# Performance work log

Measured on AMD Instinct MI355X. Metric: run time of the kernel, lower is better.

## Reference

```python
import jax, jax.numpy as jnp
import numpy as np

B, S, D, H, HD, NU, T = 64, 512, 256, 4, 64, 100000, 24


def setup_inputs() -> dict:
    key = jax.random.key(0)
    ks = jax.random.split(key, 13)
    return {
        "timeslot_embedded": jax.random.normal(ks[0], (T, D), jnp.float32),
        "user": jax.random.randint(ks[1], (B,), 0, NU, dtype=jnp.int64) if jax.config.jax_enable_x64 else jax.random.randint(ks[1], (B,), 0, NU, dtype=jnp.int32),
        "hour": jax.random.randint(ks[2], (B, S), 0, T, dtype=jnp.int32),
        "hour_mask": jax.random.randint(ks[3], (B, S, T), 0, 2, dtype=jnp.int32),
        "user_pref": jax.random.normal(ks[4], (NU, D), jnp.float32) * 0.02,
        "Wq": jax.random.normal(ks[5], (H, HD, 2 * D), jnp.float32) * 0.02,
        "bq": jnp.zeros((H, HD), jnp.float32),
        "Wk": jax.random.normal(ks[6], (H, HD, D), jnp.float32) * 0.02,
        "bk": jnp.zeros((H, HD), jnp.float32),
        "Wv": jax.random.normal(ks[7], (H, HD, D), jnp.float32) * 0.02,
        "bv": jnp.zeros((H, HD), jnp.float32),
        "Wu": jax.random.normal(ks[8], (D, D), jnp.float32) * 0.02,
        "bu": jnp.zeros((D,), jnp.float32),
    }


def reference(timeslot_embedded, user, hour, hour_mask, user_pref,
              Wq, bq, Wk, bk, Wv, bv, Wu, bu):
    b, s = hour.shape
    n = b * s
    # per-token features
    user_feat = jnp.broadcast_to(user_pref[user][:, None, :], (b, s, D)).reshape(n, D)
    time_feat = timeslot_embedded[hour.reshape(n)]          # [N, D]
    query = jnp.concatenate([user_feat, time_feat], axis=-1)  # [N, 2D]
    # all heads at once (equivalent to the per-head Linear loop)
    q = jnp.einsum('nd,hkd->nhk', query, Wq) + bq[None]               # [N, H, HD]
    k = jnp.einsum('td,hkd->htk', timeslot_embedded, Wk) + bk[:, None, :]  # [H, T, HD]
    v = jnp.einsum('td,hkd->htk', timeslot_embedded, Wv) + bv[:, None, :]  # [H, T, HD]
    scale = 1.0 / np.sqrt(HD).astype(np.float32)
    scores = jnp.einsum('nhk,htk->nht', q, k) * scale                 # [N, H, T]
    mask = hour_mask.reshape(n, T)[:, None, :]                        # [N, 1, T]
    scores = jnp.where(mask == 1, -jnp.inf, scores)
    attn = jax.nn.softmax(scores, axis=-1)
    out = jnp.einsum('nht,htk->nhk', attn, v).reshape(n, H * HD)      # concat heads
    out = out @ Wu.T + bu
    return out.reshape(b, s, D)
```

## Files before the change

kernel.cpp:

```cpp
#include <hip/hip_runtime.h>
#include <hip/hip_bf16.h>

#define QU_OFF   0
#define QT_OFF   16384
#define KK_OFF   22528
#define VV_OFF   28672
#define EU_OFF   34816
#define ET_OFF   40960
#define VWB_OFF  43264

typedef __attribute__((ext_vector_type(8))) short bf16x8;
typedef __attribute__((ext_vector_type(4))) float f32x4;

__device__ __forceinline__ unsigned short f2bf(float f) {
    unsigned u = __builtin_bit_cast(unsigned, f);
    return (unsigned short)((u + 0x7FFFu + ((u >> 16) & 1u)) >> 16);
}

__global__ __launch_bounds__(256) void precompA(
    const float* __restrict__ ts, const int* __restrict__ user,
    const float* __restrict__ user_pref,
    const float* __restrict__ Wq, const float* __restrict__ bq,
    const float* __restrict__ Wk, const float* __restrict__ bk,
    const float* __restrict__ Wv, const float* __restrict__ bv,
    float* __restrict__ ws)
{
    int tid = threadIdx.x;
    int lane = tid & 63;
    int gw = blockIdx.x * 4 + (tid >> 6);
    const float* wrow; const float* x; float bias = 0.f; float* outp;
    if (gw < 16384) {
        int b = gw >> 8, j = gw & 255;
        wrow = Wq + j * 512;
        x = user_pref + (long long)user[b] * 256;
        outp = ws + QU_OFF + gw;
    } else if (gw < 22528) {
        int r = gw - 16384, t = r >> 8, j = r & 255;
        wrow = Wq + j * 512 + 256; x = ts + t * 256; bias = bq[j];
        outp = ws + QT_OFF + r;
    } else if (gw < 28672) {
        int r = gw - 22528, t = r >> 8, j = r & 255;
        wrow = Wk + j * 256; x = ts + t * 256; bias = bk[j];
        outp = ws + KK_OFF + ((j >> 6) * 24 + t) * 64 + (j & 63);
    } else {
        int r = gw - 28672, t = r >> 8, j = r & 255;
        wrow = Wv + j * 256; x = ts + t * 256; bias = bv[j];
        outp = ws + VV_OFF + ((j >> 6) * 24 + t) * 64 + (j & 63);
    }
    float s = 0.f;
    #pragma unroll
    for (int i = 0; i < 4; ++i) s = fmaf(wrow[lane + 64 * i], x[lane + 64 * i], s);
    #pragma unroll
    for (int off = 32; off; off >>= 1) s += __shfl_xor(s, off);
    if (lane == 0) *outp = s + bias;
}

__global__ __launch_bounds__(256) void precompB(float* __restrict__ ws,
                                                const float* __restrict__ Wu)
{
    const float* qu = ws + QU_OFF;
    const float* qt = ws + QT_OFF;
    const float* kk = ws + KK_OFF;
    const float* vv = ws + VV_OFF;
    int o = blockIdx.x * 256 + threadIdx.x;
    if (o < 12288) {
        int htp = o >> 8, d = o & 255;
        int ht = htp * 2;
        int h = ht / 24;
        const float4* v0 = (const float4*)(vv + ht * 64);
        const float4* v1 = (const float4*)(vv + ht * 64 + 64);
        const float4* wp = (const float4*)(Wu + d * 256 + h * 64);
        float s0 = 0.f, s1 = 0.f;
        #pragma unroll
        for (int i = 0; i < 16; ++i) {
            float4 wv = wp[i], a = v0[i], c = v1[i];
            s0 = fmaf(a.x, wv.x, fmaf(a.y, wv.y, fmaf(a.z, wv.z, fmaf(a.w, wv.w, s0))));
            s1 = fmaf(c.x, wv.x, fmaf(c.y, wv.y, fmaf(c.z, wv.z, fmaf(c.w, wv.w, s1))));
        }
        int kt = ht >> 5, nt = d >> 4, lg = (ht >> 3) & 3, jh = (ht & 7) >> 1;
        unsigned pack = (unsigned)f2bf(s0) | ((unsigned)f2bf(s1) << 16);
        ((unsigned*)(ws + VWB_OFF))[(kt * 16 + nt) * 256 + ((d & 15) + 16 * lg) * 4 + jh] = pack;
    } else if (o < 18432) {
        int o2 = o - 12288;
        int b = o2 / 96, rem = o2 - b * 96;
        const float* qp = qu + b * 256 + (rem / 24) * 64;
        const float* kp = kk + rem * 64;
        float s = 0.f;
        #pragma unroll 8
        for (int hd = 0; hd < 64; ++hd) s = fmaf(qp[hd], kp[hd], s);
        ws[EU_OFF + o2] = expf(s * 0.125f);
    } else if (o < 20736) {
        int o3 = o - 18432;
        int tp = o3 / 96, rem = o3 - tp * 96;
        const float* qp = qt + tp * 256 + (rem / 24) * 64;
        const float* kp = kk + rem * 64;
        float s = 0.f;
        #pragma unroll 8
        for (int hd = 0; hd < 64; ++hd) s = fmaf(qp[hd], kp[hd], s);
        ws[ET_OFF + o3] = expf(s * 0.125f);
    }
}

__global__ __launch_bounds__(256) void attn_mfma(
    const int* __restrict__ hour, const int* __restrict__ hour_mask,
    const float* __restrict__ ws, const float* __restrict__ bu,
    float* __restrict__ out)
{
    const float* EU = ws + EU_OFF;
    const float* ET = ws + ET_OFF;
    __shared__ int4 A_lds[12 * 64];
    int tid = threadIdx.x;
    int nb = blockIdx.x * 64;
    int b = nb >> 9;
    {
        int tok = tid >> 2, h = tid & 3;
        int n = nb + tok;
        int th = hour[n];
        const float4* EUp = (const float4*)(EU + b * 96 + h * 24);
        const float4* ETp = (const float4*)(ET + th * 96 + h * 24);
        const int4*   mp  = (const int4*)(hour_mask + (long long)n * 24);
        float p[24]; float ssum = 0.f;
        #pragma unroll
        for (int q = 0; q < 6; ++q) {
            float4 e = EUp[q]; float4 f = ETp[q]; int4 m = mp[q];
            float v0 = (m.x != 0) ? 0.f : e.x * f.x;
            float v1 = (m.y != 0) ? 0.f : e.y * f.y;
            float v2 = (m.z != 0) ? 0.f : e.z * f.z;
            float v3 = (m.w != 0) ? 0.f : e.w * f.w;
            p[q*4+0] = v0; p[q*4+1] = v1; p[q*4+2] = v2; p[q*4+3] = v3;
            ssum += (v0 + v1) + (v2 + v3);
        }
        float r = 1.0f / ssum;
        int mt = tok >> 4, tl = tok & 15;
        #pragma unroll
        for (int tp = 0; tp < 12; ++tp) {
            int ht = h * 24 + tp * 2;
            unsigned pack = (unsigned)f2bf(p[tp*2] * r)
                          | ((unsigned)f2bf(p[tp*2+1] * r) << 16);
            int kt = ht >> 5, lg = (ht >> 3) & 3, jh = (ht & 7) >> 1;
            ((unsigned*)A_lds)[((kt * 4 + mt) * 64 + tl + 16 * lg) * 4 + jh] = pack;
        }
    }
    __syncthreads();
    int w = tid >> 6, l = tid & 63;
    const int4* Bg = (const int4*)(ws + VWB_OFF);
    bf16x8 afr[3][4], bfr[3][4];
    #pragma unroll
    for (int kt = 0; kt < 3; ++kt)
        #pragma unroll
        for (int q = 0; q < 4; ++q) {
            afr[kt][q] = __builtin_bit_cast(bf16x8, A_lds[(kt * 4 + q) * 64 + l]);
            bfr[kt][q] = __builtin_bit_cast(bf16x8, Bg[(kt * 16 + w * 4 + q) * 64 + l]);
        }
    f32x4 acc[4][4];
    #pragma unroll
    for (int mt = 0; mt < 4; ++mt)
        #pragma unroll
        for (int q = 0; q < 4; ++q) acc[mt][q] = (f32x4)0.f;
    #pragma unroll
    for (int kt = 0; kt < 3; ++kt)
        #pragma unroll
        for (int mt = 0; mt < 4; ++mt)
            #pragma unroll
            for (int q = 0; q < 4; ++q)
                acc[mt][q] = __builtin_amdgcn_mfma_f32_16x16x32_bf16(
                    afr[kt][mt], bfr[kt][q], acc[mt][q], 0, 0, 0);
    int colb = w * 64 + (l & 15);
    float buv[4];
    #pragma unroll
    for (int q = 0; q < 4; ++q) buv[q] = bu[colb + q * 16];
    int row0 = nb + (l >> 4) * 4;
    #pragma unroll
    for (int mt = 0; mt < 4; ++mt)
        #pragma unroll
        for (int q = 0; q < 4; ++q) {
            float* op = out + (size_t)(row0 + mt * 16) * 256 + colb + q * 16;
            #pragma unroll
            for (int r = 0; r < 4; ++r)
                op[(size_t)r * 256] = acc[mt][q][r] + buv[q];
        }
}

extern "C" void kernel_launch(void* const* d_in, const int* in_sizes, int n_in,
                              void* d_out, int out_size, void* d_ws, size_t ws_size,
                              hipStream_t stream)
{
    const float* ts        = (const float*)d_in[0];
    const int*   user      = (const int*)  d_in[1];
    const int*   hour      = (const int*)  d_in[2];
    const int*   hour_mask = (const int*)  d_in[3];
    const float* user_pref = (const float*)d_in[4];
    const float* Wq        = (const float*)d_in[5];
    const float* bq        = (const float*)d_in[6];
    const float* Wk        = (const float*)d_in[7];
    const float* bk        = (const float*)d_in[8];
    const float* Wv        = (const float*)d_in[9];
    const float* bv        = (const float*)d_in[10];
    const float* Wu        = (const float*)d_in[11];
    const float* bu        = (const float*)d_in[12];
    float* ws  = (float*)d_ws;
    float* out = (float*)d_out;

    hipLaunchKernelGGL(precompA, dim3(8704), dim3(256), 0, stream,
                       ts, user, user_pref, Wq, bq, Wk, bk, Wv, bv, ws);
    hipLaunchKernelGGL(precompB, dim3(81), dim3(256), 0, stream, ws, Wu);
    hipLaunchKernelGGL(attn_mfma, dim3(512), dim3(256), 0, stream,
                       hour, hour_mask, ws, bu, out);
}
```

Measured before the change: 26.12 us.

## Fuse precompute kernels into one MFMA-based kernel and compute EU in attention

Replaces the two precompute kernels (a wave-per-dot-product projection pass over 8704 blocks and a scalar follow-up) with a single 16-block kernel. It does the Q/K/V projections and the V·Wu product with bf16 MFMA, and computes the time-query exp scores in shared memory. The user-key exp scores move into the attention kernel, where each block computes its 96 values into LDS. This removes one launch and a lot of redundant global traffic. In exchange, the projections now run on only 16 blocks at bf16 precision, and each attention block repeats the EU computation.

```diff
diff --git a/kernel.cpp b/kernel.cpp
--- a/kernel.cpp
+++ b/kernel.cpp
@@ -2,12 +2,9 @@
 #include <hip/hip_bf16.h>
 
 #define QU_OFF   0
-#define QT_OFF   16384
-#define KK_OFF   22528
-#define VV_OFF   28672
-#define EU_OFF   34816
-#define ET_OFF   40960
-#define VWB_OFF  43264
+#define KK_OFF   16384
+#define ET_OFF   22528
+#define VWB_OFF  24832
 
 typedef __attribute__((ext_vector_type(8))) short bf16x8;
 typedef __attribute__((ext_vector_type(4))) float f32x4;
@@ -16,88 +13,210 @@
     unsigned u = __builtin_bit_cast(unsigned, f);
     return (unsigned short)((u + 0x7FFFu + ((u >> 16) & 1u)) >> 16);
 }
-
-__global__ __launch_bounds__(256) void precompA(
+__device__ __forceinline__ unsigned packbf(float a, float b) {
+    return (unsigned)f2bf(a) | ((unsigned)f2bf(b) << 16);
+}
+__device__ __forceinline__ bf16x8 cvt8(float4 f0, float4 f1) {
+    int4 v = make_int4(packbf(f0.x, f0.y), packbf(f0.z, f0.w),
+                       packbf(f1.x, f1.y), packbf(f1.z, f1.w));
+    return __builtin_bit_cast(bf16x8, v);
+}
+__device__ __forceinline__ float dot4(float4 a, float4 b, float s) {
+    return fmaf(a.x, b.x, fmaf(a.y, b.y, fmaf(a.z, b.z, fmaf(a.w, b.w, s))));
+}
+
+
+__global__ __launch_bounds__(256) void precomp(
     const float* __restrict__ ts, const int* __restrict__ user,
     const float* __restrict__ user_pref,
     const float* __restrict__ Wq, const float* __restrict__ bq,
     const float* __restrict__ Wk, const float* __restrict__ bk,
     const float* __restrict__ Wv, const float* __restrict__ bv,
-    float* __restrict__ ws)
+    const float* __restrict__ Wu, float* __restrict__ ws)
 {
-    int tid = threadIdx.x;
-    int lane = tid & 63;
-    int gw = blockIdx.x * 4 + (tid >> 6);
-    const float* wrow; const float* x; float bias = 0.f; float* outp;
-    if (gw < 16384) {
-        int b = gw >> 8, j = gw & 255;
-        wrow = Wq + j * 512;
-        x = user_pref + (long long)user[b] * 256;
-        outp = ws + QU_OFF + gw;
-    } else if (gw < 22528) {
-        int r = gw - 16384, t = r >> 8, j = r & 255;
-        wrow = Wq + j * 512 + 256; x = ts + t * 256; bias = bq[j];
-        outp = ws + QT_OFF + r;
-    } else if (gw < 28672) {
-        int r = gw - 22528, t = r >> 8, j = r & 255;
-        wrow = Wk + j * 256; x = ts + t * 256; bias = bk[j];
-        outp = ws + KK_OFF + ((j >> 6) * 24 + t) * 64 + (j & 63);
-    } else {
-        int r = gw - 28672, t = r >> 8, j = r & 255;
-        wrow = Wv + j * 256; x = ts + t * 256; bias = bv[j];
-        outp = ws + VV_OFF + ((j >> 6) * 24 + t) * 64 + (j & 63);
-    }
-    float s = 0.f;
-    #pragma unroll
-    for (int i = 0; i < 4; ++i) s = fmaf(wrow[lane + 64 * i], x[lane + 64 * i], s);
-    #pragma unroll
-    for (int off = 32; off; off >>= 1) s += __shfl_xor(s, off);
-    if (lane == 0) *outp = s + bias;
-}
-
-__global__ __launch_bounds__(256) void precompB(float* __restrict__ ws,
-                                                const float* __restrict__ Wu)
-{
-    const float* qu = ws + QU_OFF;
-    const float* qt = ws + QT_OFF;
-    const float* kk = ws + KK_OFF;
-    const float* vv = ws + VV_OFF;
-    int o = blockIdx.x * 256 + threadIdx.x;
-    if (o < 12288) {
-        int htp = o >> 8, d = o & 255;
-        int ht = htp * 2;
-        int h = ht / 24;
-        const float4* v0 = (const float4*)(vv + ht * 64);
-        const float4* v1 = (const float4*)(vv + ht * 64 + 64);
-        const float4* wp = (const float4*)(Wu + d * 256 + h * 64);
-        float s0 = 0.f, s1 = 0.f;
-        #pragma unroll
-        for (int i = 0; i < 16; ++i) {
-            float4 wv = wp[i], a = v0[i], c = v1[i];
-            s0 = fmaf(a.x, wv.x, fmaf(a.y, wv.y, fmaf(a.z, wv.z, fmaf(a.w, wv.w, s0))));
-            s1 = fmaf(c.x, wv.x, fmaf(c.y, wv.y, fmaf(c.z, wv.z, fmaf(c.w, wv.w, s1))));
-        }
-        int kt = ht >> 5, nt = d >> 4, lg = (ht >> 3) & 3, jh = (ht & 7) >> 1;
-        unsigned pack = (unsigned)f2bf(s0) | ((unsigned)f2bf(s1) << 16);
-        ((unsigned*)(ws + VWB_OFF))[(kt * 16 + nt) * 256 + ((d & 15) + 16 * lg) * 4 + jh] = pack;
-    } else if (o < 18432) {
-        int o2 = o - 12288;
-        int b = o2 / 96, rem = o2 - b * 96;
-        const float* qp = qu + b * 256 + (rem / 24) * 64;
-        const float* kp = kk + rem * 64;
-        float s = 0.f;
-        #pragma unroll 8
-        for (int hd = 0; hd < 64; ++hd) s = fmaf(qp[hd], kp[hd], s);
-        ws[EU_OFF + o2] = expf(s * 0.125f);
-    } else if (o < 20736) {
-        int o3 = o - 18432;
-        int tp = o3 / 96, rem = o3 - tp * 96;
-        const float* qp = qt + tp * 256 + (rem / 24) * 64;
-        const float* kp = kk + rem * 64;
-        float s = 0.f;
-        #pragma unroll 8
-        for (int hd = 0; hd < 64; ++hd) s = fmaf(qp[hd], kp[hd], s);
-        ws[ET_OFF + o3] = expf(s * 0.125f);
+    __shared__ unsigned sA[4096];
+    __shared__ float sM1[32 * 68];
+    __shared__ float sM2[32 * 68];
+    int tid = threadIdx.x, blk = blockIdx.x;
+    int w = tid >> 6, l = tid & 63;
+    int eo = (l >> 4) * 8;
+
+    if (blk < 8) {
+        int q = blk >> 1, nh = blk & 1, b0 = q * 16;
+        for (int u = tid; u < 512; u += 256) {
+            int r = u >> 5, e0 = (u & 31) * 8;
+            const float* src = user_pref + (size_t)user[b0 + r] * 256 + e0;
+            float4 f0 = *(const float4*)src, f1 = *(const float4*)(src + 4);
+            unsigned* dst = &sA[(((e0 >> 5) * 2) * 64 + (r & 15) + 16 * ((e0 >> 3) & 3)) * 4];
+            dst[0] = packbf(f0.x, f0.y); dst[1] = packbf(f0.z, f0.w);
+            dst[2] = packbf(f1.x, f1.y); dst[3] = packbf(f1.z, f1.w);
+        }
+        __syncthreads();
+        #pragma unroll
+        for (int ntq = 0; ntq < 2; ++ntq) {
+            int col = nh * 128 + (w * 2 + ntq) * 16 + (l & 15);
+            float4 fb[8][2];
+            #pragma unroll
+            for (int kt = 0; kt < 8; ++kt) {
+                const float* Bp = Wq + (size_t)col * 512 + kt * 32 + eo;
+                fb[kt][0] = *(const float4*)Bp; fb[kt][1] = *(const float4*)(Bp + 4);
+            }
+            f32x4 acc = (f32x4)0.f;
+            #pragma unroll
+            for (int kt = 0; kt < 8; ++kt) {
+                bf16x8 afr = __builtin_bit_cast(bf16x8, *(const int4*)&sA[((kt * 2) * 64 + l) * 4]);
+                acc = __builtin_amdgcn_mfma_f32_16x16x32_bf16(afr, cvt8(fb[kt][0], fb[kt][1]), acc, 0, 0, 0);
+            }
+            int row = (l >> 4) * 4;
+            #pragma unroll
+            for (int r = 0; r < 4; ++r)
+                ws[QU_OFF + (size_t)(b0 + row + r) * 256 + col] = acc[r];
+        }
+        return;
+    }
+
+    for (int u = tid; u < 768; u += 256) {
+        int r = u >> 5, e0 = (u & 31) * 8;
+        const float* src = ts + r * 256 + e0;
+        float4 f0 = *(const float4*)src, f1 = *(const float4*)(src + 4);
+        unsigned* dst = &sA[(((e0 >> 5) * 2 + (r >> 4)) * 64 + (r & 15) + 16 * ((e0 >> 3) & 3)) * 4];
+        dst[0] = packbf(f0.x, f0.y); dst[1] = packbf(f0.z, f0.w);
+        dst[2] = packbf(f1.x, f1.y); dst[3] = packbf(f1.z, f1.w);
+    }
+    __syncthreads();
+
+    if (blk < 12) {
+        int h = blk - 8;
+        int j = h * 64 + w * 16 + (l & 15);
+        float4 fa[8][2], fc[8][2];
+        #pragma unroll
+        for (int kt = 0; kt < 8; ++kt) {
+            const float* Bq = Wq + (size_t)j * 512 + 256 + kt * 32 + eo;
+            const float* Bk = Wk + (size_t)j * 256 + kt * 32 + eo;
+            fa[kt][0] = *(const float4*)Bq; fa[kt][1] = *(const float4*)(Bq + 4);
+            fc[kt][0] = *(const float4*)Bk; fc[kt][1] = *(const float4*)(Bk + 4);
+        }
+        f32x4 aca[2] = {(f32x4)0.f, (f32x4)0.f};
+        f32x4 acb[2] = {(f32x4)0.f, (f32x4)0.f};
+        #pragma unroll
+        for (int kt = 0; kt < 8; ++kt) {
+            bf16x8 bq8 = cvt8(fa[kt][0], fa[kt][1]);
+            bf16x8 bk8 = cvt8(fc[kt][0], fc[kt][1]);
+            #pragma unroll
+            for (int mt = 0; mt < 2; ++mt) {
+                bf16x8 afr = __builtin_bit_cast(bf16x8, *(const int4*)&sA[((kt * 2 + mt) * 64 + l) * 4]);
+                aca[mt] = __builtin_amdgcn_mfma_f32_16x16x32_bf16(afr, bq8, aca[mt], 0, 0, 0);
+                acb[mt] = __builtin_amdgcn_mfma_f32_16x16x32_bf16(afr, bk8, acb[mt], 0, 0, 0);
+            }
+        }
+        float bqv = bq[j], bkv = bk[j];
+        int hd = w * 16 + (l & 15);
+        #pragma unroll
+        for (int mt = 0; mt < 2; ++mt) {
+            int t0 = mt * 16 + (l >> 4) * 4;
+            #pragma unroll
+            for (int r = 0; r < 4; ++r) {
+                int t = t0 + r;
+                if (t < 24) {
+                    sM1[t * 68 + hd] = aca[mt][r] + bqv;
+                    float kv = acb[mt][r] + bkv;
+                    sM2[t * 68 + hd] = kv;
+                    ws[KK_OFF + (h * 24 + t) * 64 + hd] = kv;
+                }
+            }
+        }
+        __syncthreads();
+        for (int u = tid; u < 576; u += 256) {
+            int tp = u / 24, t = u - tp * 24;
+            const float4* qp4 = (const float4*)&sM1[tp * 68];
+            const float4* kp4 = (const float4*)&sM2[t * 68];
+            float s = 0.f;
+            #pragma unroll
+            for (int i = 0; i < 16; ++i) s = dot4(qp4[i], kp4[i], s);
+            ws[ET_OFF + tp * 96 + h * 24 + t] = expf(s * 0.125f);
+        }
+        return;
+    }
+
+    {
+        int h = blk - 12;
+        int jv = h * 64 + w * 16 + (l & 15);
+        float4 fv[8][2];
+        #pragma unroll
+        for (int kt = 0; kt < 8; ++kt) {
+            const float* Bv = Wv + (size_t)jv * 256 + kt * 32 + eo;
+            fv[kt][0] = *(const float4*)Bv; fv[kt][1] = *(const float4*)(Bv + 4);
+        }
+        f32x4 acv[2] = {(f32x4)0.f, (f32x4)0.f};
+        #pragma unroll
+        for (int kt = 0; kt < 8; ++kt) {
+            bf16x8 bv8 = cvt8(fv[kt][0], fv[kt][1]);
+            #pragma unroll
+            for (int mt = 0; mt < 2; ++mt) {
+                bf16x8 afr = __builtin_bit_cast(bf16x8, *(const int4*)&sA[((kt * 2 + mt) * 64 + l) * 4]);
+                acv[mt] = __builtin_amdgcn_mfma_f32_16x16x32_bf16(afr, bv8, acv[mt], 0, 0, 0);
+            }
+        }
+        float bvv = bv[jv];
+        int hd = w * 16 + (l & 15);
+        #pragma unroll
+        for (int mt = 0; mt < 2; ++mt) {
+            int t0 = mt * 16 + (l >> 4) * 4;
+            #pragma unroll
+            for (int r = 0; r < 4; ++r)
+                if (t0 + r < 24) sM1[(t0 + r) * 68 + hd] = acv[mt][r] + bvv;
+        }
+        __syncthreads();
+        f32x4 ac2[2][4];
+        #pragma unroll
+        for (int mt = 0; mt < 2; ++mt)
+            #pragma unroll
+            for (int q = 0; q < 4; ++q) ac2[mt][q] = (f32x4)0.f;
+        #pragma unroll
+        for (int kt2 = 0; kt2 < 2; ++kt2) {
+            int k0 = kt2 * 32 + eo;
+            bf16x8 a2[2];
+            #pragma unroll
+            for (int mt = 0; mt < 2; ++mt) {
+                int m = mt * 16 + (l & 15);
+                float4 g0 = *(const float4*)&sM1[m * 68 + k0];
+                float4 g1 = *(const float4*)&sM1[m * 68 + k0 + 4];
+                a2[mt] = cvt8(g0, g1);
+            }
+            float4 fu[4][2];
+            #pragma unroll
+            for (int q = 0; q < 4; ++q) {
+                int d = (w * 4 + q) * 16 + (l & 15);
+                const float* Bu = Wu + (size_t)d * 256 + h * 64 + k0;
+                fu[q][0] = *(const float4*)Bu; fu[q][1] = *(const float4*)(Bu + 4);
+            }
+            #pragma unroll
+            for (int q = 0; q < 4; ++q) {
+                bf16x8 bu8 = cvt8(fu[q][0], fu[q][1]);
+                #pragma unroll
+                for (int mt = 0; mt < 2; ++mt)
+                    ac2[mt][q] = __builtin_amdgcn_mfma_f32_16x16x32_bf16(a2[mt], bu8, ac2[mt][q], 0, 0, 0);
+            }
+        }
+        unsigned* vwb = (unsigned*)(ws + VWB_OFF);
+        #pragma unroll
+        for (int mt = 0; mt < 2; ++mt) {
+            int t0 = mt * 16 + (l >> 4) * 4;
+            if (t0 < 24) {
+                #pragma unroll
+                for (int q = 0; q < 4; ++q) {
+                    int d = (w * 4 + q) * 16 + (l & 15);
+                    #pragma unroll
+                    for (int pp = 0; pp < 2; ++pp) {
+                        int ht = h * 24 + t0 + pp * 2;
+                        unsigned pk = packbf(ac2[mt][q][pp * 2], ac2[mt][q][pp * 2 + 1]);
+                        int ktC = ht >> 5, ntC = d >> 4;
+                        int lgC = (ht >> 3) & 3, jhC = (ht & 7) >> 1;
+                        vwb[(ktC * 16 + ntC) * 256 + ((d & 15) + 16 * lgC) * 4 + jhC] = pk;
+                    }
+                }
+            }
+        }
     }
 }
 
@@ -106,17 +225,26 @@
     const float* __restrict__ ws, const float* __restrict__ bu,
     float* __restrict__ out)
 {
-    const float* EU = ws + EU_OFF;
     const float* ET = ws + ET_OFF;
     __shared__ int4 A_lds[12 * 64];
+    __shared__ float EU_s[96];
     int tid = threadIdx.x;
     int nb = blockIdx.x * 64;
     int b = nb >> 9;
+    if (tid < 96) {
+        const float4* qp = (const float4*)(ws + QU_OFF + b * 256 + (tid / 24) * 64);
+        const float4* kp = (const float4*)(ws + KK_OFF + tid * 64);
+        float s = 0.f;
+        #pragma unroll
+        for (int i = 0; i < 16; ++i) s = dot4(qp[i], kp[i], s);
+        EU_s[tid] = expf(s * 0.125f);
+    }
+    __syncthreads();
     {
         int tok = tid >> 2, h = tid & 3;
         int n = nb + tok;
         int th = hour[n];
-        const float4* EUp = (const float4*)(EU + b * 96 + h * 24);
+        const float4* EUp = (const float4*)(EU_s + h * 24);
         const float4* ETp = (const float4*)(ET + th * 96 + h * 24);
         const int4*   mp  = (const int4*)(hour_mask + (long long)n * 24);
         float p[24]; float ssum = 0.f;
@@ -135,8 +263,7 @@
         #pragma unroll
         for (int tp = 0; tp < 12; ++tp) {
             int ht = h * 24 + tp * 2;
-            unsigned pack = (unsigned)f2bf(p[tp*2] * r)
-                          | ((unsigned)f2bf(p[tp*2+1] * r) << 16);
+            unsigned pack = packbf(p[tp*2] * r, p[tp*2+1] * r);
             int kt = ht >> 5, lg = (ht >> 3) & 3, jh = (ht & 7) >> 1;
             ((unsigned*)A_lds)[((kt * 4 + mt) * 64 + tl + 16 * lg) * 4 + jh] = pack;
         }
@@ -201,9 +328,8 @@
     float* ws  = (float*)d_ws;
     float* out = (float*)d_out;
 
-    hipLaunchKernelGGL(precompA, dim3(8704), dim3(256), 0, stream,
-                       ts, user, user_pref, Wq, bq, Wk, bk, Wv, bv, ws);
-    hipLaunchKernelGGL(precompB, dim3(81), dim3(256), 0, stream, ws, Wu);
+    hipLaunchKernelGGL(precomp, dim3(16), dim3(256), 0, stream,
+                       ts, user, user_pref, Wq, bq, Wk, bk, Wv, bv, Wu, ws);
     hipLaunchKernelGGL(attn_mfma, dim3(512), dim3(256), 0, stream,
                        hour, hour_mask, ws, bu, out);
 }
```

Result: faster. 24.65 us (-5.6%).
